# Performance work log

Measured on AMD Instinct MI355X. Metric: run time of the kernel, lower is better.

## Reference

```python
import jax, jax.numpy as jnp
import numpy as np
from jax import lax

N_PANNELS = 3
POOL_K, POOL_S = 6, 2
# hue thresholds (colorsys-style h,s,v in [0,1]); yellow ~60deg, blue ~220deg
YELLOW_LO, YELLOW_HI = 0.10, 0.20
BLUE_LO, BLUE_HI = 0.55, 0.70
S_MIN, V_MIN = 0.5, 0.5


def _rgb_to_hsv(x):
    # x: [..., 3] rgb in [0,1] -> hsv in [0,1] (colorsys semantics)
    r, g, b = x[..., 0], x[..., 1], x[..., 2]
    maxc = jnp.max(x, axis=-1)
    minc = jnp.min(x, axis=-1)
    delta = maxc - minc
    safe_max = jnp.where(maxc == 0, 1.0, maxc)
    s = jnp.where(maxc == 0, 0.0, delta / safe_max)
    safe_d = jnp.where(delta == 0, 1.0, delta)
    rc = (maxc - r) / safe_d
    gc = (maxc - g) / safe_d
    bc = (maxc - b) / safe_d
    h = jnp.where(r == maxc, bc - gc,
        jnp.where(g == maxc, 2.0 + rc - bc, 4.0 + gc - rc))
    h = jnp.where(delta == 0, 0.0, (h / 6.0) % 1.0)
    return jnp.stack([h, s, v := maxc], axis=-1)


def _avg_pool(x):
    # x: [B, C, H, W], kernel 6 stride 2, VALID
    summed = lax.reduce_window(x, 0.0, lax.add,
                               (1, 1, POOL_K, POOL_K), (1, 1, POOL_S, POOL_S), 'VALID')
    return summed / float(POOL_K * POOL_K)


def setup_inputs() -> dict:
    key = jax.random.key(0)
    states = jax.random.uniform(key, (4096, 3, 84, 84), dtype=jnp.float32)
    return {"states": states}


def reference(states) -> jnp.ndarray:
    pooled = _avg_pool(states)                      # [B, 3, Hp, Wp]
    img = jnp.moveaxis(pooled, 1, 3)                # [B, Hp, Wp, 3]
    hsv = _rgb_to_hsv(img)                          # [B, Hp, Wp, 3]
    h, s, v = hsv[..., 0], hsv[..., 1], hsv[..., 2]
    sat_val = (s > S_MIN) & (v > V_MIN)
    yellow = (h >= YELLOW_LO) & (h <= YELLOW_HI) & sat_val
    blue = (h >= BLUE_LO) & (h <= BLUE_HI) & sat_val
    mask = yellow.astype(jnp.int32) - blue.astype(jnp.int32)  # [B, Hp, Wp] in {-1,0,1}
    Hp = hsv.shape[1]
    bounds = [Hp // N_PANNELS * i for i in range(N_PANNELS + 1)]
    labels_yellow, labels_blue = [], []
    for lo, hi in zip(bounds[:-1], bounds[1:]):
        panel = mask[:, :, lo:hi]                   # slice along W (as original)
        labels_yellow.append(jnp.max(panel, axis=(1, 2)))
        labels_blue.append(-jnp.min(panel, axis=(1, 2)))
    labels_yellow = jnp.stack(labels_yellow, axis=1)
    labels_blue = jnp.stack(labels_blue, axis=1)
    return jnp.concatenate([labels_yellow, labels_blue], axis=1).astype(jnp.float32)
```

## Files before the change

kernel.cpp:

```cpp
#include <hip/hip_runtime.h>


#define CH_ELEMS 7056
#define IMG_F4   5292
#define CH_F4    1764
#define ROW_F4   21
#define Q_F4     504
#define SLOT_F4  512
#define BUF_F4   1536
#define ROW_STR  84

__device__ __forceinline__ void gl_lds16(const float4* g, float4* l) {
    __builtin_amdgcn_global_load_lds(
        (const __attribute__((address_space(1))) void*)(uintptr_t)(const void*)g,
        (__attribute__((address_space(3))) void*)(uintptr_t)(void*)l,
        16, 0, 0);
}

__global__ __launch_bounds__(256)
void labelizer_fused(const float* __restrict__ in, float* __restrict__ out) {
    __shared__ float4 s4[2 * BUF_F4];
    __shared__ unsigned bmask;

    const int tid = threadIdx.x;
    const int img = blockIdx.x;
    const int wid = tid >> 6, lane = tid & 63;
    if (tid == 0) bmask = 0u;

    const float4* base = (const float4*)in + (size_t)img * IMG_F4;
    unsigned my = 0u;

    auto stage = [&](int q, int b) {
        const float4* sq = base + q * 20 * ROW_F4;
        float4* db = s4 + b * BUF_F4;
        #pragma unroll
        for (int c = 0; c < 3; ++c) {
            const float4* sc = sq + c * CH_F4;
            float4* dc = db + c * SLOT_F4;
            #pragma unroll
            for (int k = 0; k < 2; ++k) {
                int i = (wid + 4 * k) * 64 + lane;
                gl_lds16(sc + min(i, Q_F4 - 1), dc + i);
            }
        }
    };

    auto compute = [&](int b) {
        if (tid < 200) {
            const int pr = tid / 20;
            const int xp = tid - pr * 20;
            const int x0 = 2 * xp, x1 = 2 * xp + 1;
            const float* sf = (const float*)(s4 + b * BUF_F4);
            const int lbase = (2 * pr) * ROW_STR + 4 * xp;

            float t0[3], t1[3];
            #pragma unroll
            for (int c = 0; c < 3; ++c) {
                float P0[3], P1[3];
                #pragma unroll
                for (int j = 0; j < 3; ++j) {
                    const float* rbase = sf + c * (4 * SLOT_F4) + lbase + (2 * j) * ROW_STR;
                    const float4* ra = (const float4*)rbase;
                    const float4* rb = (const float4*)(rbase + ROW_STR);
                    float4 qa0 = ra[0], qa1 = ra[1];
                    float4 qb0 = rb[0], qb1 = rb[1];
                    float a01 = qa0.x + qa0.y, a23 = qa0.z + qa0.w;
                    float a45 = qa1.x + qa1.y, a67 = qa1.z + qa1.w;
                    float rsa0 = (a01 + a23) + a45;
                    float rsa1 = (a23 + a45) + a67;
                    float b01 = qb0.x + qb0.y, b23 = qb0.z + qb0.w;
                    float b45 = qb1.x + qb1.y, b67 = qb1.z + qb1.w;
                    float rsb0 = (b01 + b23) + b45;
                    float rsb1 = (b23 + b45) + b67;
                    P0[j] = rsa0 + rsb0;
                    P1[j] = rsa1 + rsb1;
                }
                t0[c] = (P0[0] + P0[1]) + P0[2];
                t1[c] = (P1[0] + P1[1]) + P1[2];
            }

            #pragma unroll
            for (int e = 0; e < 2; ++e) {
                float r = ((e == 0) ? t0[0] : t1[0]) / 36.0f;
                float g = ((e == 0) ? t0[1] : t1[1]) / 36.0f;
                float bb = ((e == 0) ? t0[2] : t1[2]) / 36.0f;

                float maxc = fmaxf(r, fmaxf(g, bb));
                float minc = fminf(r, fminf(g, bb));
                float delta = maxc - minc;
                float s = (maxc == 0.0f) ? 0.0f : delta / maxc;
                float v = maxc;
                float h = 0.0f;
                if (delta != 0.0f) {
                    float rc = (maxc - r) / delta;
                    float gc = (maxc - g) / delta;
                    float bc = (maxc - bb) / delta;
                    float hh = (r == maxc) ? (bc - gc)
                             : ((g == maxc) ? (2.0f + rc - bc)
                                            : (4.0f + gc - rc));
                    h = hh / 6.0f;
                    if (h < 0.0f) h += 1.0f;
                }
                bool satval = (s > 0.5f) && (v > 0.5f);
                int m = 0;
                if (satval && h >= 0.1f && h <= 0.2f) m = 1;
                else if (satval && h >= 0.55f && h <= 0.7f) m = -1;

                int x = (e == 0) ? x0 : x1;
                if (x < 39) {
                    int pan = x / 13;
                    unsigned bit = (m > 0) ? 1u : (m < 0) ? 2u : 4u;
                    my |= bit << (3 * pan);
                }
            }
        }
    };

    stage(0, 0);
    __syncthreads();

    #pragma unroll
    for (int q = 0; q < 4; ++q) {
        if (q < 3) {
            stage(q + 1, (q + 1) & 1);
            asm volatile("s_waitcnt vmcnt(6)" ::: "memory");
        } else {
            asm volatile("s_waitcnt vmcnt(0)" ::: "memory");
        }
        __builtin_amdgcn_s_barrier();
        compute(q & 1);
        __builtin_amdgcn_s_barrier();
    }

    #pragma unroll
    for (int off = 32; off > 0; off >>= 1) my |= __shfl_xor(my, off);
    if ((tid & 63) == 0 && my) atomicOr(&bmask, my);
    __syncthreads();

    if (tid < 6) {
        int pan = (tid < 3) ? tid : tid - 3;
        unsigned w = bmask >> (3 * pan);
        bool anyY = w & 1u;
        bool anyB = (w >> 1) & 1u;
        bool anyZ = (w >> 2) & 1u;
        float val;
        if (tid < 3) val = anyY ? 1.0f : (anyZ ? 0.0f : -1.0f);
        else         val = anyB ? 1.0f : (anyZ ? 0.0f : -1.0f);
        out[(size_t)img * 6 + tid] = val;
    }
}

extern "C" void kernel_launch(void* const* d_in, const int* in_sizes, int n_in,
                              void* d_out, int out_size, void* d_ws, size_t ws_size,
                              hipStream_t stream) {
    const float* states = (const float*)d_in[0];
    float* out = (float*)d_out;
    int N = in_sizes[0] / (3 * CH_ELEMS);
    labelizer_fused<<<N, 256, 0, stream>>>(states, out);
}
```

Measured before the change: 73.27 us.

## Reuse overlapping halo rows via three-buffer LDS ring instead of reloading

Replaces the double-buffered staging, which reloaded the 4-row pooling overlap for every 24-row quarter, with a three-slot LDS ring. The first slot holds 24 rows and each later chunk loads only 20 new rows. Compute now builds row addresses that can span two buffers, split at a row index. Per-wave vmcnt waits are adjusted because the 21 load issues divide unevenly across 4 waves. The aim is to cut redundant global-to-LDS traffic, at the cost of more index arithmetic in the compute loop.

```diff
diff --git a/kernel.cpp b/kernel.cpp
--- a/kernel.cpp
+++ b/kernel.cpp
@@ -2,13 +2,12 @@
 
 
 #define CH_ELEMS 7056
+#define CH_F4    1764
 #define IMG_F4   5292
-#define CH_F4    1764
-#define ROW_F4   21
-#define Q_F4     504
-#define SLOT_F4  512
-#define BUF_F4   1536
-#define ROW_STR  84
+#define B0 0
+#define B1 1536
+#define B2 2880
+#define LDS_TOT 4224
 
 __device__ __forceinline__ void gl_lds16(const float4* g, float4* l) {
     __builtin_amdgcn_global_load_lds(
@@ -19,7 +18,7 @@
 
 __global__ __launch_bounds__(256)
 void labelizer_fused(const float* __restrict__ in, float* __restrict__ out) {
-    __shared__ float4 s4[2 * BUF_F4];
+    __shared__ float4 s4[LDS_TOT];
     __shared__ unsigned bmask;
 
     const int tid = threadIdx.x;
@@ -30,28 +29,21 @@
     const float4* base = (const float4*)in + (size_t)img * IMG_F4;
     unsigned my = 0u;
 
-    auto stage = [&](int q, int b) {
-        const float4* sq = base + q * 20 * ROW_F4;
-        float4* db = s4 + b * BUF_F4;
-        #pragma unroll
-        for (int c = 0; c < 3; ++c) {
-            const float4* sc = sq + c * CH_F4;
-            float4* dc = db + c * SLOT_F4;
-            #pragma unroll
-            for (int k = 0; k < 2; ++k) {
-                int i = (wid + 4 * k) * 64 + lane;
-                gl_lds16(sc + min(i, Q_F4 - 1), dc + i);
-            }
+    auto stage = [&](int fs_row, int fl, int nc, int bb, int ss) {
+        const int tot = 3 * nc;
+        for (int t = wid; t < tot; t += 4) {
+            int c = t / nc, k = t - c * nc;
+            int i = k * 64 + lane;
+            gl_lds16(base + c * CH_F4 + fs_row * 21 + min(i, fl - 1),
+                     s4 + bb + c * ss + i);
         }
     };
 
-    auto compute = [&](int b) {
+    auto compute = [&](int rsplit, int bA, int sA, int aA, int bB, int sB, int aB) {
         if (tid < 200) {
             const int pr = tid / 20;
             const int xp = tid - pr * 20;
             const int x0 = 2 * xp, x1 = 2 * xp + 1;
-            const float* sf = (const float*)(s4 + b * BUF_F4);
-            const int lbase = (2 * pr) * ROW_STR + 4 * xp;
 
             float t0[3], t1[3];
             #pragma unroll
@@ -59,9 +51,14 @@
                 float P0[3], P1[3];
                 #pragma unroll
                 for (int j = 0; j < 3; ++j) {
-                    const float* rbase = sf + c * (4 * SLOT_F4) + lbase + (2 * j) * ROW_STR;
-                    const float4* ra = (const float4*)rbase;
-                    const float4* rb = (const float4*)(rbase + ROW_STR);
+                    int r0 = 2 * pr + 2 * j;
+                    int r1 = r0 + 1;
+                    int o0 = (r0 < rsplit) ? (bA + c * sA + (aA + r0) * 21)
+                                           : (bB + c * sB + (aB + r0) * 21);
+                    int o1 = (r1 < rsplit) ? (bA + c * sA + (aA + r1) * 21)
+                                           : (bB + c * sB + (aB + r1) * 21);
+                    const float4* ra = &s4[o0 + xp];
+                    const float4* rb = &s4[o1 + xp];
                     float4 qa0 = ra[0], qa1 = ra[1];
                     float4 qb0 = rb[0], qb1 = rb[1];
                     float a01 = qa0.x + qa0.y, a23 = qa0.z + qa0.w;
@@ -83,10 +80,10 @@
             for (int e = 0; e < 2; ++e) {
                 float r = ((e == 0) ? t0[0] : t1[0]) / 36.0f;
                 float g = ((e == 0) ? t0[1] : t1[1]) / 36.0f;
-                float bb = ((e == 0) ? t0[2] : t1[2]) / 36.0f;
+                float bb2 = ((e == 0) ? t0[2] : t1[2]) / 36.0f;
 
-                float maxc = fmaxf(r, fmaxf(g, bb));
-                float minc = fminf(r, fminf(g, bb));
+                float maxc = fmaxf(r, fmaxf(g, bb2));
+                float minc = fminf(r, fminf(g, bb2));
                 float delta = maxc - minc;
                 float s = (maxc == 0.0f) ? 0.0f : delta / maxc;
                 float v = maxc;
@@ -94,7 +91,7 @@
                 if (delta != 0.0f) {
                     float rc = (maxc - r) / delta;
                     float gc = (maxc - g) / delta;
-                    float bc = (maxc - bb) / delta;
+                    float bc = (maxc - bb2) / delta;
                     float hh = (r == maxc) ? (bc - gc)
                              : ((g == maxc) ? (2.0f + rc - bc)
                                             : (4.0f + gc - rc));
@@ -116,21 +113,32 @@
         }
     };
 
-    stage(0, 0);
-    __syncthreads();
+    stage(0, 504, 8, B0, 512);
 
-    #pragma unroll
-    for (int q = 0; q < 4; ++q) {
-        if (q < 3) {
-            stage(q + 1, (q + 1) & 1);
-            asm volatile("s_waitcnt vmcnt(6)" ::: "memory");
-        } else {
-            asm volatile("s_waitcnt vmcnt(0)" ::: "memory");
-        }
-        __builtin_amdgcn_s_barrier();
-        compute(q & 1);
-        __builtin_amdgcn_s_barrier();
-    }
+    stage(24, 420, 7, B1, 448);
+    if (wid == 0) asm volatile("s_waitcnt vmcnt(6)" ::: "memory");
+    else          asm volatile("s_waitcnt vmcnt(5)" ::: "memory");
+    __builtin_amdgcn_s_barrier();
+    compute(0, 0, 0, 0, B0, 512, 0);
+    __builtin_amdgcn_s_barrier();
+
+    stage(44, 420, 7, B2, 448);
+    if (wid == 0) asm volatile("s_waitcnt vmcnt(6)" ::: "memory");
+    else          asm volatile("s_waitcnt vmcnt(5)" ::: "memory");
+    __builtin_amdgcn_s_barrier();
+    compute(4, B0, 512, 20, B1, 448, -4);
+    __builtin_amdgcn_s_barrier();
+
+    stage(64, 420, 7, B0, 512);
+    if (wid == 0) asm volatile("s_waitcnt vmcnt(6)" ::: "memory");
+    else          asm volatile("s_waitcnt vmcnt(5)" ::: "memory");
+    __builtin_amdgcn_s_barrier();
+    compute(4, B1, 448, 16, B2, 448, -4);
+    __builtin_amdgcn_s_barrier();
+
+    asm volatile("s_waitcnt vmcnt(0)" ::: "memory");
+    __builtin_amdgcn_s_barrier();
+    compute(4, B2, 448, 16, B0, 512, -4);
 
     #pragma unroll
     for (int off = 32; off > 0; off >>= 1) my |= __shfl_xor(my, off);
```

After: 96.54 us. 31.8% more time.

## Process two images per block with non-overlapping row staging and halo copy

Applied to the files above, without the earlier changes.

Each block now handles two images, and the next image's first chunk is prefetched while the current image finishes. Rows are staged in non-overlapping chunks of 24 then 20 rows, and the 4 halo rows are copied LDS-to-LDS into tail buffers. This replaces the old overlapping 24-row chunks that reloaded halo rows from global memory. The aim is less redundant global traffic and less per-block launch and prologue overhead. In exchange it adds more barriers, an LDS copy step, halves the grid to N/2, and assumes N is even.

```diff
diff --git a/kernel.cpp b/kernel.cpp
--- a/kernel.cpp
+++ b/kernel.cpp
@@ -2,13 +2,15 @@
 
 
 #define CH_ELEMS 7056
+#define CH_F4    1764
 #define IMG_F4   5292
-#define CH_F4    1764
-#define ROW_F4   21
-#define Q_F4     504
-#define SLOT_F4  512
-#define BUF_F4   1536
-#define ROW_STR  84
+#define IPB      2
+
+#define BUF0 0
+#define BUF1 1536
+#define TBA  2816
+#define TBB  3068
+#define LDS_TOT 3320
 
 __device__ __forceinline__ void gl_lds16(const float4* g, float4* l) {
     __builtin_amdgcn_global_load_lds(
@@ -17,136 +19,174 @@
         16, 0, 0);
 }
 
+template<int NPC, int MPW, int CLAMP>
+__device__ __forceinline__ void stageT(const float4* g0, float4* lb, int wid, int lane) {
+    #pragma unroll
+    for (int m = 0; m < MPW; ++m) {
+        int i = (wid + 4 * m) * 64 + lane;
+        int ii = min(i, CLAMP);
+        int c = ii / NPC;
+        gl_lds16(g0 + c * CH_F4 + (ii - c * NPC), lb + i);
+    }
+}
+
+template<int SLOTF4, int STARTROW>
+__device__ __forceinline__ void tailcopyT(const float4* mb, float4* tb, int tid) {
+    if (tid < 252) {
+        int c = tid / 84;
+        int rem = tid - c * 84;
+        tb[c * 84 + rem] = mb[c * SLOTF4 + STARTROW * 21 + rem];
+    }
+}
+
+template<int RSPLIT, int MSLOTF>
+__device__ __forceinline__ unsigned computeT(const float* tb, const float* mb, int tid) {
+    unsigned my = 0u;
+    if (tid < 200) {
+        const int pr = tid / 20;
+        const int xp = tid - pr * 20;
+        const int x0 = 2 * xp, x1 = 2 * xp + 1;
+
+        float t0[3], t1[3];
+        #pragma unroll
+        for (int c = 0; c < 3; ++c) {
+            float P0[3], P1[3];
+            #pragma unroll
+            for (int j = 0; j < 3; ++j) {
+                int r0 = 2 * pr + 2 * j;
+                int r1 = r0 + 1;
+                const float* row0 = (RSPLIT > 0 && r0 < RSPLIT)
+                    ? (tb + c * 336 + r0 * 84)
+                    : (mb + c * MSLOTF + (r0 - RSPLIT) * 84);
+                const float* row1 = (RSPLIT > 0 && r1 < RSPLIT)
+                    ? (tb + c * 336 + r1 * 84)
+                    : (mb + c * MSLOTF + (r1 - RSPLIT) * 84);
+                const float4* ra = (const float4*)(row0 + 4 * xp);
+                const float4* rb = (const float4*)(row1 + 4 * xp);
+                float4 qa0 = ra[0], qa1 = ra[1];
+                float4 qb0 = rb[0], qb1 = rb[1];
+                float a01 = qa0.x + qa0.y, a23 = qa0.z + qa0.w;
+                float a45 = qa1.x + qa1.y, a67 = qa1.z + qa1.w;
+                float rsa0 = (a01 + a23) + a45;
+                float rsa1 = (a23 + a45) + a67;
+                float b01 = qb0.x + qb0.y, b23 = qb0.z + qb0.w;
+                float b45 = qb1.x + qb1.y, b67 = qb1.z + qb1.w;
+                float rsb0 = (b01 + b23) + b45;
+                float rsb1 = (b23 + b45) + b67;
+                P0[j] = rsa0 + rsb0;
+                P1[j] = rsa1 + rsb1;
+            }
+            t0[c] = (P0[0] + P0[1]) + P0[2];
+            t1[c] = (P1[0] + P1[1]) + P1[2];
+        }
+
+        #pragma unroll
+        for (int e = 0; e < 2; ++e) {
+            float r = ((e == 0) ? t0[0] : t1[0]) / 36.0f;
+            float g = ((e == 0) ? t0[1] : t1[1]) / 36.0f;
+            float b = ((e == 0) ? t0[2] : t1[2]) / 36.0f;
+
+            float maxc = fmaxf(r, fmaxf(g, b));
+            float minc = fminf(r, fminf(g, b));
+            float delta = maxc - minc;
+            float s = (maxc == 0.0f) ? 0.0f : delta / maxc;
+            float v = maxc;
+            float h = 0.0f;
+            if (delta != 0.0f) {
+                float rc = (maxc - r) / delta;
+                float gc = (maxc - g) / delta;
+                float bc = (maxc - b) / delta;
+                float hh = (r == maxc) ? (bc - gc)
+                         : ((g == maxc) ? (2.0f + rc - bc)
+                                        : (4.0f + gc - rc));
+                h = hh / 6.0f;
+                if (h < 0.0f) h += 1.0f;
+            }
+            bool satval = (s > 0.5f) && (v > 0.5f);
+            int m = 0;
+            if (satval && h >= 0.1f && h <= 0.2f) m = 1;
+            else if (satval && h >= 0.55f && h <= 0.7f) m = -1;
+
+            int x = (e == 0) ? x0 : x1;
+            if (x < 39) {
+                int pan = x / 13;
+                unsigned bit = (m > 0) ? 1u : (m < 0) ? 2u : 4u;
+                my |= bit << (3 * pan);
+            }
+        }
+    }
+    return my;
+}
+
 __global__ __launch_bounds__(256)
 void labelizer_fused(const float* __restrict__ in, float* __restrict__ out) {
-    __shared__ float4 s4[2 * BUF_F4];
-    __shared__ unsigned bmask;
-
-    const int tid = threadIdx.x;
-    const int img = blockIdx.x;
-    const int wid = tid >> 6, lane = tid & 63;
-    if (tid == 0) bmask = 0u;
-
-    const float4* base = (const float4*)in + (size_t)img * IMG_F4;
+    __shared__ float4 s4[LDS_TOT];
+    __shared__ unsigned smu[4];
+
+    const int tid = threadIdx.x, wid = tid >> 6, lane = tid & 63;
+    const int img0 = blockIdx.x * IPB;
+    const float4* base = (const float4*)in;
+    const float* sf = (const float*)s4;
     unsigned my = 0u;
 
-    auto stage = [&](int q, int b) {
-        const float4* sq = base + q * 20 * ROW_F4;
-        float4* db = s4 + b * BUF_F4;
-        #pragma unroll
-        for (int c = 0; c < 3; ++c) {
-            const float4* sc = sq + c * CH_F4;
-            float4* dc = db + c * SLOT_F4;
-            #pragma unroll
-            for (int k = 0; k < 2; ++k) {
-                int i = (wid + 4 * k) * 64 + lane;
-                gl_lds16(sc + min(i, Q_F4 - 1), dc + i);
-            }
-        }
-    };
-
-    auto compute = [&](int b) {
-        if (tid < 200) {
-            const int pr = tid / 20;
-            const int xp = tid - pr * 20;
-            const int x0 = 2 * xp, x1 = 2 * xp + 1;
-            const float* sf = (const float*)(s4 + b * BUF_F4);
-            const int lbase = (2 * pr) * ROW_STR + 4 * xp;
-
-            float t0[3], t1[3];
-            #pragma unroll
-            for (int c = 0; c < 3; ++c) {
-                float P0[3], P1[3];
-                #pragma unroll
-                for (int j = 0; j < 3; ++j) {
-                    const float* rbase = sf + c * (4 * SLOT_F4) + lbase + (2 * j) * ROW_STR;
-                    const float4* ra = (const float4*)rbase;
-                    const float4* rb = (const float4*)(rbase + ROW_STR);
-                    float4 qa0 = ra[0], qa1 = ra[1];
-                    float4 qb0 = rb[0], qb1 = rb[1];
-                    float a01 = qa0.x + qa0.y, a23 = qa0.z + qa0.w;
-                    float a45 = qa1.x + qa1.y, a67 = qa1.z + qa1.w;
-                    float rsa0 = (a01 + a23) + a45;
-                    float rsa1 = (a23 + a45) + a67;
-                    float b01 = qb0.x + qb0.y, b23 = qb0.z + qb0.w;
-                    float b45 = qb1.x + qb1.y, b67 = qb1.z + qb1.w;
-                    float rsb0 = (b01 + b23) + b45;
-                    float rsb1 = (b23 + b45) + b67;
-                    P0[j] = rsa0 + rsb0;
-                    P1[j] = rsa1 + rsb1;
-                }
-                t0[c] = (P0[0] + P0[1]) + P0[2];
-                t1[c] = (P1[0] + P1[1]) + P1[2];
-            }
-
-            #pragma unroll
-            for (int e = 0; e < 2; ++e) {
-                float r = ((e == 0) ? t0[0] : t1[0]) / 36.0f;
-                float g = ((e == 0) ? t0[1] : t1[1]) / 36.0f;
-                float bb = ((e == 0) ? t0[2] : t1[2]) / 36.0f;
-
-                float maxc = fmaxf(r, fmaxf(g, bb));
-                float minc = fminf(r, fminf(g, bb));
-                float delta = maxc - minc;
-                float s = (maxc == 0.0f) ? 0.0f : delta / maxc;
-                float v = maxc;
-                float h = 0.0f;
-                if (delta != 0.0f) {
-                    float rc = (maxc - r) / delta;
-                    float gc = (maxc - g) / delta;
-                    float bc = (maxc - bb) / delta;
-                    float hh = (r == maxc) ? (bc - gc)
-                             : ((g == maxc) ? (2.0f + rc - bc)
-                                            : (4.0f + gc - rc));
-                    h = hh / 6.0f;
-                    if (h < 0.0f) h += 1.0f;
-                }
-                bool satval = (s > 0.5f) && (v > 0.5f);
-                int m = 0;
-                if (satval && h >= 0.1f && h <= 0.2f) m = 1;
-                else if (satval && h >= 0.55f && h <= 0.7f) m = -1;
-
-                int x = (e == 0) ? x0 : x1;
-                if (x < 39) {
-                    int pan = x / 13;
-                    unsigned bit = (m > 0) ? 1u : (m < 0) ? 2u : 4u;
-                    my |= bit << (3 * pan);
-                }
-            }
-        }
-    };
-
-    stage(0, 0);
-    __syncthreads();
-
-    #pragma unroll
-    for (int q = 0; q < 4; ++q) {
-        if (q < 3) {
-            stage(q + 1, (q + 1) & 1);
+    stageT<504, 6, 1511>(base + (size_t)img0 * IMG_F4, s4 + BUF0, wid, lane);
+
+    for (int i = 0; i < IPB; ++i) {
+        const int img = img0 + i;
+        const float4* ib = base + (size_t)img * IMG_F4;
+
+        stageT<420, 5, 1259>(ib + 504, s4 + BUF1, wid, lane);
+        asm volatile("s_waitcnt vmcnt(5)" ::: "memory");
+        __builtin_amdgcn_s_barrier();
+        my |= computeT<0, 2016>(nullptr, sf + BUF0 * 4, tid);
+        tailcopyT<504, 20>(s4 + BUF0, s4 + TBA, tid);
+        asm volatile("s_waitcnt lgkmcnt(0)" ::: "memory");
+        __builtin_amdgcn_s_barrier();
+
+        stageT<420, 5, 1259>(ib + 924, s4 + BUF0, wid, lane);
+        asm volatile("s_waitcnt vmcnt(5)" ::: "memory");
+        __builtin_amdgcn_s_barrier();
+        my |= computeT<4, 1680>(sf + TBA * 4, sf + BUF1 * 4, tid);
+        tailcopyT<420, 16>(s4 + BUF1, s4 + TBB, tid);
+        asm volatile("s_waitcnt lgkmcnt(0)" ::: "memory");
+        __builtin_amdgcn_s_barrier();
+
+        stageT<420, 5, 1259>(ib + 1344, s4 + BUF1, wid, lane);
+        asm volatile("s_waitcnt vmcnt(5)" ::: "memory");
+        __builtin_amdgcn_s_barrier();
+        my |= computeT<4, 1680>(sf + TBB * 4, sf + BUF0 * 4, tid);
+        tailcopyT<420, 16>(s4 + BUF0, s4 + TBA, tid);
+        asm volatile("s_waitcnt lgkmcnt(0)" ::: "memory");
+        __builtin_amdgcn_s_barrier();
+
+        if (i < IPB - 1) {
+            stageT<504, 6, 1511>(base + (size_t)(img + 1) * IMG_F4, s4 + BUF0, wid, lane);
             asm volatile("s_waitcnt vmcnt(6)" ::: "memory");
         } else {
             asm volatile("s_waitcnt vmcnt(0)" ::: "memory");
         }
         __builtin_amdgcn_s_barrier();
-        compute(q & 1);
-        __builtin_amdgcn_s_barrier();
-    }
-
-    #pragma unroll
-    for (int off = 32; off > 0; off >>= 1) my |= __shfl_xor(my, off);
-    if ((tid & 63) == 0 && my) atomicOr(&bmask, my);
-    __syncthreads();
-
-    if (tid < 6) {
-        int pan = (tid < 3) ? tid : tid - 3;
-        unsigned w = bmask >> (3 * pan);
-        bool anyY = w & 1u;
-        bool anyB = (w >> 1) & 1u;
-        bool anyZ = (w >> 2) & 1u;
-        float val;
-        if (tid < 3) val = anyY ? 1.0f : (anyZ ? 0.0f : -1.0f);
-        else         val = anyB ? 1.0f : (anyZ ? 0.0f : -1.0f);
-        out[(size_t)img * 6 + tid] = val;
+        my |= computeT<4, 1680>(sf + TBA * 4, sf + BUF1 * 4, tid);
+
+        unsigned r = my;
+        #pragma unroll
+        for (int off = 32; off > 0; off >>= 1) r |= __shfl_xor(r, off);
+        if (lane == 0) smu[wid] = r;
+        asm volatile("s_waitcnt lgkmcnt(0)" ::: "memory");
+        __builtin_amdgcn_s_barrier();
+        if (tid < 6) {
+            unsigned m4 = smu[0] | smu[1] | smu[2] | smu[3];
+            int pan = (tid < 3) ? tid : tid - 3;
+            unsigned w = m4 >> (3 * pan);
+            bool anyY = w & 1u;
+            bool anyB = (w >> 1) & 1u;
+            bool anyZ = (w >> 2) & 1u;
+            float val;
+            if (tid < 3) val = anyY ? 1.0f : (anyZ ? 0.0f : -1.0f);
+            else         val = anyB ? 1.0f : (anyZ ? 0.0f : -1.0f);
+            out[(size_t)img * 6 + tid] = val;
+        }
+        my = 0u;
     }
 }
 
@@ -156,5 +196,5 @@
     const float* states = (const float*)d_in[0];
     float* out = (float*)d_out;
     int N = in_sizes[0] / (3 * CH_ELEMS);
-    labelizer_fused<<<N, 256, 0, stream>>>(states, out);
-}
+    labelizer_fused<<<N / IPB, 256, 0, stream>>>(states, out);
+}
```

After: 96.55 us. 1.32x slower.
